# Kernel optimization log

Measured on AMD Instinct MI355X. Metric: run time of the kernel, lower is better.

## Reference

```python
import jax, jax.numpy as jnp
import numpy as np

M = 8192          # tokens (batch*seq)
K = 4096          # in_features
N = 4096          # out_features
BK = 64           # block_k (row_block of B)
BN = 64           # block_n (col_block of B)
NR = K // BK      # 64 block rows of B
NC = N // BN      # 64 block cols of B
OCC = 4           # nonzero blocks per column (and per row)
TB = NR * OCC     # total nonzero blocks = 256


def _build_indices():
    # Regular block mask: each column has OCC nonzero block-rows, each row has OCC
    # nonzero block-cols (matches BlockMask.regular invariants). Deterministic
    # construction: column c uses rows (c + s*(NR//OCC)) % NR, sorted ascending.
    step = NR // OCC
    cols = np.arange(NC)
    rows = np.sort((cols[None, :] + step * np.arange(OCC)[:, None]) % NR, axis=0)  # [OCC, NC]
    # _build_data_indices assigns data slots column-major, row-ascending within a
    # column, so column c's blocks (sorted by row) get slots c*OCC + s.
    data = cols[None, :] * OCC + np.arange(OCC)[:, None]  # [OCC, NC]
    return rows.astype(np.int32), data.astype(np.int32)


def setup_inputs() -> dict:
    key = jax.random.key(0)
    k1, k2 = jax.random.split(key)
    rows, data = _build_indices()
    return {
        "A": jax.random.normal(k1, (M, K), dtype=jnp.float32),
        "B_data": jax.random.normal(k2, (BK, BN * TB), dtype=jnp.float32) * 0.02,
        "row_indices": jnp.asarray(rows),
        "data_indices": jnp.asarray(data),
    }


def reference(A, B_data, row_indices, data_indices):
    # A: [M, K]; B_data: [BK, BN*TB]; indices: [OCC, NC]
    m, k = A.shape
    occ, nc = row_indices.shape
    bk = B_data.shape[0]
    tb = occ * nc
    bn = B_data.shape[1] // tb
    nr = k // bk
    # Gather A blocks per (sub_k, out_col): [m, occ, nc, bk]
    A_blocks = A.reshape(m, nr, bk)[:, row_indices]
    # Gather B blocks: B_data laid out as [bk, tb, bn] -> [tb, bk, bn] -> [occ, nc, bk, bn]
    B_blocks = jnp.transpose(B_data.reshape(bk, tb, bn), (1, 0, 2))[data_indices]
    # Accumulate over occ and bk (fp32 accumulation like the Triton kernel)
    C = jnp.einsum('mock,ockn->mcn', A_blocks, B_blocks,
                   preferred_element_type=jnp.float32)
    return C.reshape(m, nc * bn).astype(A.dtype)
```

## Files before the change

kernel.cpp:

```cpp
#include <hip/hip_runtime.h>
#include <hip/hip_bf16.h>

typedef __bf16 bf16x8 __attribute__((ext_vector_type(8)));
typedef float  f32x4  __attribute__((ext_vector_type(4)));

__device__ __forceinline__ void dma16(const float* g, float* l) {
    typedef const __attribute__((address_space(1))) unsigned int* gp_t;
    typedef __attribute__((address_space(3))) unsigned int*       lp_t;
    __builtin_amdgcn_global_load_lds((gp_t)(const void*)g, (lp_t)(void*)l, 16, 0, 0);
}

__global__ __launch_bounds__(512, 2) void sparse_linear_kernel(
    const float* __restrict__ A, const float* __restrict__ Bd,
    const int* __restrict__ rowi, const int* __restrict__ di,
    float* __restrict__ C)
{
    __shared__ __align__(16) float Aring[8][2][16 * 64];
    __shared__ __align__(16) unsigned short Bt[8 * 64 * 64];
    char* BtB = (char*)Bt;

    const int bid = blockIdx.x;
    const int cp  = bid & 31;
    const int grp = bid >> 5;
    const int t    = threadIdx.x;
    const int lane = t & 63;
    const int w    = t >> 6;

    int koff[4], dsj[2][4];
    #pragma unroll
    for (int s = 0; s < 4; ++s) {
        koff[s] = rowi[s * 64 + cp] * 64;
        dsj[0][s] = di[s * 64 + cp];
        dsj[1][s] = di[s * 64 + cp + 32];
    }

    const long wrow0 = (long)grp * 1024 + w * 64;

    auto dmaA = [&](int st, int slot) {
        if (st > 31) st = 31;
        const int q = st >> 4, mt = (st >> 2) & 3, kb = st & 3;
        float* slotp = &Aring[w][slot][0];
        #pragma unroll
        for (int i = 0; i < 4; ++i) {
            const int rr  = i * 4 + (lane >> 4);
            const int kfl = (((lane & 15) * 16) ^ (rr << 4)) >> 2;
            const float* g = A + (wrow0 + q * 512 + mt * 16 + rr) * 4096 + koff[kb] + kfl;
            dma16(g, slotp + i * 256);
        }
    };

    dmaA(0, 0);
    dmaA(1, 1);

    {
        const int jj = t >> 6;
        const int n  = t & 63;
        const float* Bg = Bd + (long)dsj[jj >> 2][jj & 3] * 64 + n;
        char* dst = BtB + jj * 8192 + n * 128;
        const int sw = (n & 7) << 4;
        #pragma unroll
        for (int k4 = 0; k4 < 16; ++k4) {
            union { ushort4 u4; __bf16 e[4]; } pk;
            pk.e[0] = (__bf16)Bg[(long)(4 * k4 + 0) * 16384];
            pk.e[1] = (__bf16)Bg[(long)(4 * k4 + 1) * 16384];
            pk.e[2] = (__bf16)Bg[(long)(4 * k4 + 2) * 16384];
            pk.e[3] = (__bf16)Bg[(long)(4 * k4 + 3) * 16384];
            *(ushort4*)(dst + ((8 * k4) ^ sw)) = pk.u4;
        }
    }
    __syncthreads();

    f32x4 acc[2][4];
    #pragma unroll
    for (int j = 0; j < 2; ++j)
        #pragma unroll
        for (int n2 = 0; n2 < 4; ++n2) acc[j][n2] = f32x4{0.f, 0.f, 0.f, 0.f};

    #pragma unroll 1
    for (int q = 0; q < 2; ++q) {
        #pragma unroll
        for (int local = 0; local < 16; ++local) {
            const int st = q * 16 + local;
            const int mt = local >> 2, kb = local & 3;
            const int slot = st & 1;

            if ((st & 3) <= 1 && st >= 4) asm volatile("s_waitcnt vmcnt(36)" ::: "memory");
            else                          asm volatile("s_waitcnt vmcnt(4)"  ::: "memory");
            __builtin_amdgcn_sched_barrier(0);

            const char* ab = (const char*)&Aring[w][slot][0];
            const int r   = lane & 15;
            const int q32 = (lane >> 4) * 32;
            f32x4 a0 = *(const f32x4*)(ab + r * 256 + ((q32)            ^ (r << 4)));
            f32x4 a1 = *(const f32x4*)(ab + r * 256 + ((q32 + 16)       ^ (r << 4)));
            f32x4 a2 = *(const f32x4*)(ab + r * 256 + ((128 + q32)      ^ (r << 4)));
            f32x4 a3 = *(const f32x4*)(ab + r * 256 + ((128 + q32 + 16) ^ (r << 4)));
            union { bf16x8 v; __bf16 e[8]; } af0, af1;
            #pragma unroll
            for (int i = 0; i < 4; ++i) {
                af0.e[i]     = (__bf16)a0[i];
                af0.e[i + 4] = (__bf16)a1[i];
                af1.e[i]     = (__bf16)a2[i];
                af1.e[i + 4] = (__bf16)a3[i];
            }

            __builtin_amdgcn_s_setprio(1);
            #pragma unroll
            for (int kh = 0; kh < 2; ++kh) {
                const bf16x8 afv = kh ? af1.v : af0.v;
                #pragma unroll
                for (int j = 0; j < 2; ++j) {
                    const char* bb = BtB + (j * 4 + kb) * 8192;
                    #pragma unroll
                    for (int n2 = 0; n2 < 4; ++n2) {
                        const int nr = n2 * 16 + (lane & 15);
                        bf16x8 bf = *(const bf16x8*)(bb + nr * 128 +
                                    ((kh * 64 + (lane >> 4) * 16) ^ ((nr & 7) << 4)));
                        acc[j][n2] = __builtin_amdgcn_mfma_f32_16x16x32_bf16(
                            afv, bf, acc[j][n2], 0, 0, 0);
                    }
                }
            }
            __builtin_amdgcn_s_setprio(0);

            dmaA(st + 2, slot);

            if (kb == 3) {
                __builtin_amdgcn_sched_barrier(0);
                const long crow0 = wrow0 + q * 512 + mt * 16 + (lane >> 4) * 4;
                #pragma unroll
                for (int j = 0; j < 2; ++j) {
                    const long col0 = (long)(cp + 32 * j) * 64 + (lane & 15);
                    #pragma unroll
                    for (int n2 = 0; n2 < 4; ++n2) {
                        #pragma unroll
                        for (int v = 0; v < 4; ++v)
                            __builtin_nontemporal_store(acc[j][n2][v],
                                &C[(crow0 + v) * 4096 + col0 + n2 * 16]);
                        acc[j][n2] = f32x4{0.f, 0.f, 0.f, 0.f};
                    }
                }
                __builtin_amdgcn_sched_barrier(0);
            }
        }
    }

    asm volatile("s_waitcnt vmcnt(0)" ::: "memory");
}

extern "C" void kernel_launch(void* const* d_in, const int* in_sizes, int n_in,
                              void* d_out, int out_size, void* d_ws, size_t ws_size,
                              hipStream_t stream) {
    const float* A    = (const float*)d_in[0];
    const float* Bd   = (const float*)d_in[1];
    const int*   rowi = (const int*)d_in[2];
    const int*   di   = (const int*)d_in[3];
    float*       C    = (float*)d_out;

    dim3 grid(8 * 32);
    dim3 block(512);
    hipLaunchKernelGGL(sparse_linear_kernel, grid, block, 0, stream,
                       A, Bd, rowi, di, C);
}
```

Before: 67.29 us.

## Swap loop order to keep B fragments in registers across M-tiles

The inner step order changes from M-tile-outer/K-block-inner to K-block-outer/M-tile-inner. Each B fragment set is then loaded from LDS once per K-block and reused across four M-tiles held in registers, instead of being re-read every step. This quadruples the accumulator register footprint (128 floats) and adds 32 bf16x8 B registers, which risks spills or lower occupancy under launch_bounds(512,2). Output stores are deferred: the first half's results are written during the second half's early steps and the rest after the loop, with the vmcnt waits retuned to match.

```diff
diff --git a/kernel.cpp b/kernel.cpp
--- a/kernel.cpp
+++ b/kernel.cpp
@@ -29,7 +29,7 @@
     int koff[4], dsj[2][4];
     #pragma unroll
     for (int s = 0; s < 4; ++s) {
-        koff[s] = rowi[s * 64 + cp] * 64;
+        koff[s]   = rowi[s * 64 + cp] * 64;
         dsj[0][s] = di[s * 64 + cp];
         dsj[1][s] = di[s * 64 + cp + 32];
     }
@@ -38,13 +38,14 @@
 
     auto dmaA = [&](int st, int slot) {
         if (st > 31) st = 31;
-        const int q = st >> 4, mt = (st >> 2) & 3, kb = st & 3;
+        const int q = st >> 4, kb = (st >> 2) & 3, mt = st & 3;
         float* slotp = &Aring[w][slot][0];
+        const long rbase = wrow0 + q * 512 + mt * 16;
         #pragma unroll
         for (int i = 0; i < 4; ++i) {
             const int rr  = i * 4 + (lane >> 4);
             const int kfl = (((lane & 15) * 16) ^ (rr << 4)) >> 2;
-            const float* g = A + (wrow0 + q * 512 + mt * 16 + rr) * 4096 + koff[kb] + kfl;
+            const float* g = A + (rbase + rr) * 4096 + koff[kb] + kfl;
             dma16(g, slotp + i * 256);
         }
     };
@@ -70,23 +71,64 @@
     }
     __syncthreads();
 
-    f32x4 acc[2][4];
+    f32x4 acc[4][2][4];
     #pragma unroll
-    for (int j = 0; j < 2; ++j)
+    for (int m = 0; m < 4; ++m)
         #pragma unroll
-        for (int n2 = 0; n2 < 4; ++n2) acc[j][n2] = f32x4{0.f, 0.f, 0.f, 0.f};
+        for (int j = 0; j < 2; ++j)
+            #pragma unroll
+            for (int n2 = 0; n2 < 4; ++n2) acc[m][j][n2] = f32x4{0.f, 0.f, 0.f, 0.f};
+
+    bf16x8 bfr[2][2][4];
 
     #pragma unroll 1
     for (int q = 0; q < 2; ++q) {
         #pragma unroll
         for (int local = 0; local < 16; ++local) {
             const int st = q * 16 + local;
-            const int mt = local >> 2, kb = local & 3;
+            const int kb = local >> 2, mt = local & 3;
             const int slot = st & 1;
 
-            if ((st & 3) <= 1 && st >= 4) asm volatile("s_waitcnt vmcnt(36)" ::: "memory");
-            else                          asm volatile("s_waitcnt vmcnt(4)"  ::: "memory");
+            if (local >= 1 && local <= 4) {
+                if (q == 1) asm volatile("s_waitcnt vmcnt(36)" ::: "memory");
+                else        asm volatile("s_waitcnt vmcnt(4)"  ::: "memory");
+            } else {
+                asm volatile("s_waitcnt vmcnt(4)" ::: "memory");
+            }
             __builtin_amdgcn_sched_barrier(0);
+
+            if (q == 1 && local < 4) {
+                const int mts = local;
+                const long crow0 = wrow0 + 0 * 512 + mts * 16 + (lane >> 4) * 4;
+                #pragma unroll
+                for (int j = 0; j < 2; ++j) {
+                    const long col0 = (long)(cp + 32 * j) * 64 + (lane & 15);
+                    #pragma unroll
+                    for (int n2 = 0; n2 < 4; ++n2) {
+                        #pragma unroll
+                        for (int v = 0; v < 4; ++v)
+                            __builtin_nontemporal_store(acc[mts][j][n2][v],
+                                &C[(crow0 + v) * 4096 + col0 + n2 * 16]);
+                        acc[mts][j][n2] = f32x4{0.f, 0.f, 0.f, 0.f};
+                    }
+                }
+            }
+
+            if ((local & 3) == 0) {
+                #pragma unroll
+                for (int j = 0; j < 2; ++j) {
+                    const char* bb = BtB + (j * 4 + kb) * 8192;
+                    #pragma unroll
+                    for (int kh = 0; kh < 2; ++kh)
+                        #pragma unroll
+                        for (int n2 = 0; n2 < 4; ++n2) {
+                            const int nr = n2 * 16 + (lane & 15);
+                            const int kbyte = kh * 64 + (lane >> 4) * 16;
+                            bfr[j][kh][n2] = *(const bf16x8*)(bb + nr * 128 +
+                                             (kbyte ^ ((nr & 7) << 4)));
+                        }
+                }
+            }
 
             const char* ab = (const char*)&Aring[w][slot][0];
             const int r   = lane & 15;
@@ -109,43 +151,33 @@
             for (int kh = 0; kh < 2; ++kh) {
                 const bf16x8 afv = kh ? af1.v : af0.v;
                 #pragma unroll
-                for (int j = 0; j < 2; ++j) {
-                    const char* bb = BtB + (j * 4 + kb) * 8192;
+                for (int j = 0; j < 2; ++j)
                     #pragma unroll
-                    for (int n2 = 0; n2 < 4; ++n2) {
-                        const int nr = n2 * 16 + (lane & 15);
-                        bf16x8 bf = *(const bf16x8*)(bb + nr * 128 +
-                                    ((kh * 64 + (lane >> 4) * 16) ^ ((nr & 7) << 4)));
-                        acc[j][n2] = __builtin_amdgcn_mfma_f32_16x16x32_bf16(
-                            afv, bf, acc[j][n2], 0, 0, 0);
-                    }
-                }
+                    for (int n2 = 0; n2 < 4; ++n2)
+                        acc[mt][j][n2] = __builtin_amdgcn_mfma_f32_16x16x32_bf16(
+                            afv, bfr[j][kh][n2], acc[mt][j][n2], 0, 0, 0);
             }
             __builtin_amdgcn_s_setprio(0);
 
             dmaA(st + 2, slot);
-
-            if (kb == 3) {
-                __builtin_amdgcn_sched_barrier(0);
-                const long crow0 = wrow0 + q * 512 + mt * 16 + (lane >> 4) * 4;
-                #pragma unroll
-                for (int j = 0; j < 2; ++j) {
-                    const long col0 = (long)(cp + 32 * j) * 64 + (lane & 15);
-                    #pragma unroll
-                    for (int n2 = 0; n2 < 4; ++n2) {
-                        #pragma unroll
-                        for (int v = 0; v < 4; ++v)
-                            __builtin_nontemporal_store(acc[j][n2][v],
-                                &C[(crow0 + v) * 4096 + col0 + n2 * 16]);
-                        acc[j][n2] = f32x4{0.f, 0.f, 0.f, 0.f};
-                    }
-                }
-                __builtin_amdgcn_sched_barrier(0);
-            }
         }
     }
 
     asm volatile("s_waitcnt vmcnt(0)" ::: "memory");
+    #pragma unroll
+    for (int mts = 0; mts < 4; ++mts) {
+        const long crow0 = wrow0 + 1 * 512 + mts * 16 + (lane >> 4) * 4;
+        #pragma unroll
+        for (int j = 0; j < 2; ++j) {
+            const long col0 = (long)(cp + 32 * j) * 64 + (lane & 15);
+            #pragma unroll
+            for (int n2 = 0; n2 < 4; ++n2)
+                #pragma unroll
+                for (int v = 0; v < 4; ++v)
+                    __builtin_nontemporal_store(acc[mts][j][n2][v],
+                        &C[(crow0 + v) * 4096 + col0 + n2 * 16]);
+        }
+    }
 }
 
 extern "C" void kernel_launch(void* const* d_in, const int* in_sizes, int n_in,
```

New measurement: 142.0 us. 111% more time.
